# Performance work log

Measured on AMD Instinct MI355X. Metric: run time of the kernel, lower is better.

## Reference

```python
import jax, jax.numpy as jnp
import numpy as np

C1, C2, C3, S = 3, 6, 3, 16
SPLITS = (9 * C1 * 1, C1, 9 * C2 * C1, C2, 9 * C3 * C2, C3, 9 * S * C3, S)  # sums to 811
B = 16384


def _channelize(w, cin, cout):
    # w: [B, cout*9*cin] -> filter [3, 3, cin, B*cout] (B-major on out axis)
    w = w.reshape(-1, cout, 9 * cin)
    w = jnp.transpose(w, (2, 0, 1))          # [9*cin, B, cout]
    return w.reshape(3, 3, cin, -1)


def _gconv(x, w, groups):
    # x: [1, H, W, B*cin], w: [3, 3, cin, B*cout]; grouped conv, groups=B
    return jax.lax.conv_general_dilated(
        x, w, window_strides=(1, 1), padding='VALID',
        dimension_numbers=('NHWC', 'HWIO', 'NHWC'),
        feature_group_count=groups)


def _maxpool2(x):
    return jax.lax.reduce_window(x, -jnp.inf, jax.lax.max,
                                 (1, 2, 2, 1), (1, 2, 2, 1), 'VALID')


def setup_inputs() -> dict:
    key = jax.random.key(0)
    ks = jax.random.split(key, 8)
    tot = sum(SPLITS)
    return {
        'image': jax.random.normal(ks[0], (1, 28, 28, B), jnp.float32),
        'state': jax.random.normal(ks[1], (B, S), jnp.float32),
        'W1': jax.random.normal(ks[2], (S, 16), jnp.float32) * 0.25,
        'b1': jnp.zeros((16,), jnp.float32),
        'W2': jax.random.normal(ks[3], (16, 16), jnp.float32) * 0.25,
        'b2': jnp.zeros((16,), jnp.float32),
        'W3': jax.random.normal(ks[4], (16, tot), jnp.float32) * 0.1,
        'b3': jnp.zeros((tot,), jnp.float32),
    }


def reference(image, state, W1, b1, W2, b2, W3, b3):
    batch = state.shape[0]
    # Hypernetwork MLP producing per-sample conv weights (dropout rate 0 => identity)
    h = jax.nn.relu(state @ W1 + b1)
    h = jax.nn.relu(h @ W2 + b2)
    w = h @ W3 + b3                               # [B, 811]
    idx = np.cumsum(SPLITS)[:-1]
    w1, bb1, w2, bb2, w3, bb3, w4, bb4 = jnp.split(w, idx, axis=1)

    x = _gconv(image, _channelize(w1, 1, C1), batch) + bb1.reshape(-1)   # [1,26,26,B*C1]
    x = _maxpool2(jax.nn.relu(x))                                        # [1,13,13,B*C1]
    x = _gconv(x, _channelize(w2, C1, C2), batch) + bb2.reshape(-1)      # [1,11,11,B*C2]
    x = _maxpool2(jax.nn.relu(x))                                        # [1,5,5,B*C2]
    x = _gconv(x, _channelize(w3, C2, C3), batch) + bb3.reshape(-1)      # [1,3,3,B*C3]
    x = jax.nn.relu(x)
    x = _gconv(x, _channelize(w4, C3, S), batch) + bb4.reshape(-1)       # [1,1,1,B*S]
    x = jnp.transpose(x, (3, 1, 2, 0)).reshape(-1, S)                    # [B, S]
    return state + x
```

## Files before the change

kernel.cpp:

```cpp
#include <hip/hip_runtime.h>

#define BLK   256
#define NSAMP 4
#define REG   1760
#define OFF_P2   0
#define OFF_P3   160
#define OFF_W    392
#define OFF_P1   1204


__device__ __forceinline__ float bf2f(unsigned short u) {
    return __uint_as_float(((unsigned int)u) << 16);
}
__device__ __forceinline__ unsigned short f2bf(float f) {
    unsigned int x = __float_as_uint(f);
    return (unsigned short)((x + 0x7fffu + ((x >> 16) & 1u)) >> 16);
}
__device__ __forceinline__ void wsync() {
    __builtin_amdgcn_wave_barrier();
    __asm__ volatile("s_waitcnt lgkmcnt(0)" ::: "memory");
    __builtin_amdgcn_wave_barrier();
}

__device__ __forceinline__ bool is_bf16(const void* p, int elems) {
    const unsigned short* h = (const unsigned short*)p;
    int n = elems; if (n > 32) n = 32;
    int nz = 0, ok = 0;
    for (int i = 0; i < n; i += 2) {
        unsigned short u = h[i];
        if (u == 0) continue;
        ++nz;
        unsigned int e = (u >> 7) & 255u;
        if (e >= 100u && e <= 141u) ++ok;
    }
    if (nz < 4) return true;
    return 4 * ok >= 3 * nz;
}

__global__ __launch_bounds__(BLK, 5)
void dyncnn4_kernel(const void* __restrict__ image,
                    const void* __restrict__ state,
                    const void* __restrict__ W1, const void* __restrict__ b1,
                    const void* __restrict__ W2, const void* __restrict__ b2,
                    const void* __restrict__ W3, const void* __restrict__ b3,
                    void* __restrict__ out,
                    int B, int nswz)
{
    __shared__ float SH[NSAMP * REG];
    __shared__ float s_st[NSAMP][16];
    __shared__ float s_h1[NSAMP][16];
    __shared__ float s_h2[NSAMP][16];

    const int t    = threadIdx.x;
    const int wv   = t >> 6;
    const int lane = t & 63;

    const bool im_bf = is_bf16(image, 784 * B);
    const bool st_bf = is_bf16(state, 16 * B);
    const bool w1_bf = is_bf16(W1, 256);
    const bool b1_bf = is_bf16(b1, 16);
    const bool w2_bf = is_bf16(W2, 256);
    const bool b2_bf = is_bf16(b2, 16);
    const bool w3_bf = is_bf16(W3, 12976);
    const bool b3_bf = is_bf16(b3, 811);
    const bool out_bf = im_bf && st_bf && w1_bf && w2_bf && w3_bf;

    int p = blockIdx.x;
    int l = (nswz > 0) ? ((p & 7) * nswz + (p >> 3)) : p;
    const int b0 = l * NSAMP;

    unsigned short* su = (unsigned short*)SH;

    if (wv == 0) {
        int s = lane >> 4, j = lane & 15;
        int gi = (b0 + s) * 16 + j;
        s_st[s][j] = st_bf ? bf2f(((const unsigned short*)state)[gi])
                           : ((const float*)state)[gi];
        wsync();
        float acc = b1_bf ? bf2f(((const unsigned short*)b1)[j])
                          : ((const float*)b1)[j];
#pragma unroll
        for (int k = 0; k < 16; ++k) {
            float w = w1_bf ? bf2f(((const unsigned short*)W1)[k * 16 + j])
                            : ((const float*)W1)[k * 16 + j];
            acc += s_st[s][k] * w;
        }
        s_h1[s][j] = fmaxf(acc, 0.f);
        wsync();
        acc = b2_bf ? bf2f(((const unsigned short*)b2)[j])
                    : ((const float*)b2)[j];
#pragma unroll
        for (int k = 0; k < 16; ++k) {
            float w = w2_bf ? bf2f(((const unsigned short*)W2)[k * 16 + j])
                            : ((const float*)W2)[k * 16 + j];
            acc += s_h1[s][k] * w;
        }
        s_h2[s][j] = fmaxf(acc, 0.f);
    } else {
        if (im_bf) {
            const unsigned short* im = (const unsigned short*)image;
            for (int pix = t - 64; pix < 784; pix += 192) {
                const uint2 v = *(const uint2*)(im + pix * B + b0);
                su[0 * 2 * REG + pix] = (unsigned short)(v.x);
                su[1 * 2 * REG + pix] = (unsigned short)(v.x >> 16);
                su[2 * 2 * REG + pix] = (unsigned short)(v.y);
                su[3 * 2 * REG + pix] = (unsigned short)(v.y >> 16);
            }
        } else {
            const float* im = (const float*)image;
            for (int pix = t - 64; pix < 784; pix += 192) {
                const float4 v = *(const float4*)(im + pix * B + b0);
                su[0 * 2 * REG + pix] = f2bf(v.x);
                su[1 * 2 * REG + pix] = f2bf(v.y);
                su[2 * 2 * REG + pix] = f2bf(v.z);
                su[3 * 2 * REG + pix] = f2bf(v.w);
            }
        }
    }
    __syncthreads();

    {
        float h2r[4][16];
        const float4* hp = (const float4*)&s_h2[0][0];
#pragma unroll
        for (int i = 0; i < 16; ++i) {
            float4 v = hp[i];
            h2r[i >> 2][(i & 3) * 4 + 0] = v.x;
            h2r[i >> 2][(i & 3) * 4 + 1] = v.y;
            h2r[i >> 2][(i & 3) * 4 + 2] = v.z;
            h2r[i >> 2][(i & 3) * 4 + 3] = v.w;
        }
        for (int j = t; j < 811; j += BLK) {
            float bb = b3_bf ? bf2f(((const unsigned short*)b3)[j])
                             : ((const float*)b3)[j];
            float a0 = bb, a1 = bb, a2 = bb, a3 = bb;
            if (w3_bf) {
                const unsigned short* q = (const unsigned short*)W3 + j;
#pragma unroll
                for (int k = 0; k < 16; ++k) {
                    float w = bf2f(q[k * 811]);
                    a0 += h2r[0][k] * w; a1 += h2r[1][k] * w;
                    a2 += h2r[2][k] * w; a3 += h2r[3][k] * w;
                }
            } else {
                const float* q = (const float*)W3 + j;
#pragma unroll
                for (int k = 0; k < 16; ++k) {
                    float w = q[k * 811];
                    a0 += h2r[0][k] * w; a1 += h2r[1][k] * w;
                    a2 += h2r[2][k] * w; a3 += h2r[3][k] * w;
                }
            }
            SH[0 * REG + OFF_W + j] = a0;
            SH[1 * REG + OFF_W + j] = a1;
            SH[2 * REG + OFF_W + j] = a2;
            SH[3 * REG + OFF_W + j] = a3;
        }
    }
    __syncthreads();

    const int sb = wv * REG;

    {
        float wc[27], cb[3];
#pragma unroll
        for (int i = 0; i < 27; ++i) wc[i] = SH[sb + OFF_W + i];
#pragma unroll
        for (int c = 0; c < 3; ++c) cb[c] = SH[sb + OFF_W + 27 + c];
        const unsigned* suw = (const unsigned*)&SH[sb];
#pragma unroll
        for (int it = 0; it < 3; ++it) {
            int pix = lane + it * 64;
            if (pix < 169) {
                int py = pix / 13, px = pix - py * 13;
                int iy = 2 * py;
                float pt[4][4];
#pragma unroll
                for (int dy = 0; dy < 4; ++dy) {
                    int r = (iy + dy) * 14 + px;
                    unsigned d0 = suw[r], d1 = suw[r + 1];
                    pt[dy][0] = __uint_as_float(d0 << 16);
                    pt[dy][1] = __uint_as_float(d0 & 0xffff0000u);
                    pt[dy][2] = __uint_as_float(d1 << 16);
                    pt[dy][3] = __uint_as_float(d1 & 0xffff0000u);
                }
                float* op = &SH[sb + OFF_P1 + py * 14 + px];
#pragma unroll
                for (int c = 0; c < 3; ++c) {
                    float a00 = 0.f, a01 = 0.f, a10 = 0.f, a11 = 0.f;
#pragma unroll
                    for (int ky = 0; ky < 3; ++ky)
#pragma unroll
                        for (int kx = 0; kx < 3; ++kx) {
                            float w = wc[c * 9 + ky * 3 + kx];
                            a00 += pt[ky][kx] * w;
                            a01 += pt[ky][kx + 1] * w;
                            a10 += pt[ky + 1][kx] * w;
                            a11 += pt[ky + 1][kx + 1] * w;
                        }
                    float m = fmaxf(fmaxf(a00, a01), fmaxf(a10, a11));
                    op[c * 182] = fmaxf(m + cb[c], 0.f);
                }
            }
        }
    }
    wsync();

    {
        int g = lane >> 5, q = lane & 31;
        if (q < 25) {
            int py = q / 5, px = q - py * 5;
            float pt[3][4][4];
#pragma unroll
            for (int ci = 0; ci < 3; ++ci)
#pragma unroll
                for (int dy = 0; dy < 4; ++dy)
#pragma unroll
                    for (int dx = 0; dx < 4; ++dx)
                        pt[ci][dy][dx] =
                            SH[sb + OFF_P1 + ci * 182 + (2 * py + dy) * 14 + 2 * px + dx];
#pragma unroll
            for (int it = 0; it < 3; ++it) {
                int c = it * 2 + g;
                float wreg[27];
                const int wo = sb + OFF_W + 30 + c * 27;
#pragma unroll
                for (int i = 0; i < 27; ++i) wreg[i] = SH[wo + i];
                float a00 = 0.f, a01 = 0.f, a10 = 0.f, a11 = 0.f;
#pragma unroll
                for (int ci = 0; ci < 3; ++ci)
#pragma unroll
                    for (int ky = 0; ky < 3; ++ky)
#pragma unroll
                        for (int kx = 0; kx < 3; ++kx) {
                            float w = wreg[(ky * 3 + kx) * 3 + ci];
                            a00 += pt[ci][ky][kx] * w;
                            a01 += pt[ci][ky][kx + 1] * w;
                            a10 += pt[ci][ky + 1][kx] * w;
                            a11 += pt[ci][ky + 1][kx + 1] * w;
                        }
                float m = fmaxf(fmaxf(a00, a01), fmaxf(a10, a11));
                SH[sb + OFF_P2 + c * 25 + q] = fmaxf(m + SH[sb + OFF_W + 192 + c], 0.f);
            }
        }
    }
    wsync();

    if (lane < 27) {
        int c = lane / 9, pq = lane - c * 9;
        int py = pq / 3, px = pq - py * 3;
        const int wo = sb + OFF_W + 198 + c * 54;
        float acc = SH[sb + OFF_W + 360 + c];
#pragma unroll
        for (int ky = 0; ky < 3; ++ky)
#pragma unroll
            for (int kx = 0; kx < 3; ++kx)
#pragma unroll
                for (int ci = 0; ci < 6; ++ci)
                    acc += SH[sb + OFF_P2 + ci * 25 + (py + ky) * 5 + px + kx] *
                           SH[wo + (ky * 3 + kx) * 6 + ci];
        SH[sb + OFF_P3 + lane] = fmaxf(acc, 0.f);
    }
    wsync();

    if (lane < 16) {
        int os = lane;
        float p3r[27];
#pragma unroll
        for (int i = 0; i < 27; ++i) p3r[i] = SH[sb + OFF_P3 + i];
        const int wo = sb + OFF_W + 363 + os * 27;
        float acc = SH[sb + OFF_W + 795 + os];
#pragma unroll
        for (int pp = 0; pp < 9; ++pp)
#pragma unroll
            for (int ci = 0; ci < 3; ++ci)
                acc += p3r[ci * 9 + pp] * SH[wo + pp * 3 + ci];
        acc += s_st[wv][os];
        int gi = (b0 + wv) * 16 + os;
        if (out_bf) ((unsigned short*)out)[gi] = f2bf(acc);
        else        ((float*)out)[gi] = acc;
    }
}

extern "C" void kernel_launch(void* const* d_in, const int* in_sizes, int n_in,
                              void* d_out, int out_size, void* d_ws, size_t ws_size,
                              hipStream_t stream) {
    (void)d_ws; (void)ws_size; (void)n_in; (void)out_size;
    int B = in_sizes[1] / 16;
    int nblocks = B / NSAMP;
    int nswz = (nblocks % 8 == 0) ? (nblocks / 8) : 0;

    dyncnn4_kernel<<<nblocks, BLK, 0, stream>>>(
        d_in[0], d_in[1], d_in[2], d_in[3], d_in[4], d_in[5], d_in[6], d_in[7],
        d_out, B, nswz);
}
```

Baseline: 158.0 us.

## Store pool1 output as bf16 to shrink LDS and raise occupancy; split conv3/conv4 across lanes

```diff
diff --git a/kernel.cpp b/kernel.cpp
--- a/kernel.cpp
+++ b/kernel.cpp
@@ -2,11 +2,11 @@
 
 #define BLK   256
 #define NSAMP 4
-#define REG   1760
+#define REG   1480
 #define OFF_P2   0
-#define OFF_P3   160
+#define OFF_P3   152
 #define OFF_W    392
-#define OFF_P1   1204
+#define HW_P1    2408
 
 
 __device__ __forceinline__ float bf2f(unsigned short u) {
@@ -37,7 +37,7 @@
     return 4 * ok >= 3 * nz;
 }
 
-__global__ __launch_bounds__(BLK, 5)
+__global__ __launch_bounds__(BLK, 6)
 void dyncnn4_kernel(const void* __restrict__ image,
                     const void* __restrict__ state,
                     const void* __restrict__ W1, const void* __restrict__ b1,
@@ -184,7 +184,7 @@
                     pt[dy][2] = __uint_as_float(d1 << 16);
                     pt[dy][3] = __uint_as_float(d1 & 0xffff0000u);
                 }
-                float* op = &SH[sb + OFF_P1 + py * 14 + px];
+                unsigned short* op = &su[sb * 2 + HW_P1 + py * 14 + px];
 #pragma unroll
                 for (int c = 0; c < 3; ++c) {
                     float a00 = 0.f, a01 = 0.f, a10 = 0.f, a11 = 0.f;
@@ -199,7 +199,7 @@
                             a11 += pt[ky + 1][kx + 1] * w;
                         }
                     float m = fmaxf(fmaxf(a00, a01), fmaxf(a10, a11));
-                    op[c * 182] = fmaxf(m + cb[c], 0.f);
+                    op[c * 182] = f2bf(fmaxf(m + cb[c], 0.f));
                 }
             }
         }
@@ -210,15 +210,19 @@
         int g = lane >> 5, q = lane & 31;
         if (q < 25) {
             int py = q / 5, px = q - py * 5;
+            const unsigned* p1w = (const unsigned*)&SH[sb + 1204];
             float pt[3][4][4];
 #pragma unroll
             for (int ci = 0; ci < 3; ++ci)
 #pragma unroll
-                for (int dy = 0; dy < 4; ++dy)
-#pragma unroll
-                    for (int dx = 0; dx < 4; ++dx)
-                        pt[ci][dy][dx] =
-                            SH[sb + OFF_P1 + ci * 182 + (2 * py + dy) * 14 + 2 * px + dx];
+                for (int dy = 0; dy < 4; ++dy) {
+                    int r = ci * 91 + (2 * py + dy) * 7 + px;
+                    unsigned d0 = p1w[r], d1 = p1w[r + 1];
+                    pt[ci][dy][0] = __uint_as_float(d0 << 16);
+                    pt[ci][dy][1] = __uint_as_float(d0 & 0xffff0000u);
+                    pt[ci][dy][2] = __uint_as_float(d1 << 16);
+                    pt[ci][dy][3] = __uint_as_float(d1 & 0xffff0000u);
+                }
 #pragma unroll
             for (int it = 0; it < 3; ++it) {
                 int c = it * 2 + g;
@@ -246,39 +250,48 @@
     }
     wsync();
 
-    if (lane < 27) {
-        int c = lane / 9, pq = lane - c * 9;
-        int py = pq / 3, px = pq - py * 3;
-        const int wo = sb + OFF_W + 198 + c * 54;
-        float acc = SH[sb + OFF_W + 360 + c];
-#pragma unroll
-        for (int ky = 0; ky < 3; ++ky)
-#pragma unroll
-            for (int kx = 0; kx < 3; ++kx)
-#pragma unroll
-                for (int ci = 0; ci < 6; ++ci)
-                    acc += SH[sb + OFF_P2 + ci * 25 + (py + ky) * 5 + px + kx] *
-                           SH[wo + (ky * 3 + kx) * 6 + ci];
-        SH[sb + OFF_P3 + lane] = fmaxf(acc, 0.f);
+    {
+        float acc = 0.f;
+        int pq = lane % 27;
+        int half = lane / 27;
+        int c = pq / 9, pos = pq - c * 9;
+        int py = pos / 3, px = pos - py * 3;
+        if (lane < 54) {
+            const int wo = sb + OFF_W + 198 + c * 54;
+            const int cb3 = half * 3;
+#pragma unroll
+            for (int ky = 0; ky < 3; ++ky)
+#pragma unroll
+                for (int kx = 0; kx < 3; ++kx)
+#pragma unroll
+                    for (int ci = 0; ci < 3; ++ci)
+                        acc += SH[sb + OFF_P2 + (cb3 + ci) * 25 + (py + ky) * 5 + px + kx] *
+                               SH[wo + (ky * 3 + kx) * 6 + cb3 + ci];
+        }
+        float other = __shfl(acc, (lane + 27) & 63);
+        if (lane < 27)
+            SH[sb + OFF_P3 + pq] = fmaxf(acc + other + SH[sb + OFF_W + 360 + c], 0.f);
     }
     wsync();
 
-    if (lane < 16) {
-        int os = lane;
-        float p3r[27];
-#pragma unroll
-        for (int i = 0; i < 27; ++i) p3r[i] = SH[sb + OFF_P3 + i];
-        const int wo = sb + OFF_W + 363 + os * 27;
-        float acc = SH[sb + OFF_W + 795 + os];
-#pragma unroll
-        for (int pp = 0; pp < 9; ++pp)
-#pragma unroll
-            for (int ci = 0; ci < 3; ++ci)
-                acc += p3r[ci * 9 + pp] * SH[wo + pp * 3 + ci];
-        acc += s_st[wv][os];
-        int gi = (b0 + wv) * 16 + os;
-        if (out_bf) ((unsigned short*)out)[gi] = f2bf(acc);
-        else        ((float*)out)[gi] = acc;
+    {
+        float acc = 0.f;
+        int os = lane & 15, h = (lane >> 4) & 1;
+        if (lane < 32) {
+            const int wo = sb + OFF_W + 363 + os * 27;
+            int p0 = h ? 4 : 0, p1 = h ? 9 : 4;
+            for (int pp = p0; pp < p1; ++pp)
+#pragma unroll
+                for (int ci = 0; ci < 3; ++ci)
+                    acc += SH[sb + OFF_P3 + ci * 9 + pp] * SH[wo + pp * 3 + ci];
+        }
+        float other = __shfl(acc, (lane + 16) & 63);
+        if (lane < 16) {
+            float tot = acc + other + SH[sb + OFF_W + 795 + os] + s_st[wv][os];
+            int gi = (b0 + wv) * 16 + os;
+            if (out_bf) ((unsigned short*)out)[gi] = f2bf(tot);
+            else        ((float*)out)[gi] = tot;
+        }
     }
 }
 
```

Measured after the change: 207.2 us. 1.31x slower.
